# Kernel optimization log

Measured on AMD Instinct MI355X. Metric: run time of the kernel, lower is better.

Reference implementation:

```python
import jax, jax.numpy as jnp
import numpy as np
from jax import lax

DN = ('NCHW', 'OIHW', 'NCHW')

def _attn(x, w):
    # x: [B, C, H, W]; channel pool -> [B, 2, H, W]
    pool = jnp.concatenate([x.max(axis=1, keepdims=True), x.mean(axis=1, keepdims=True)], axis=1)
    g = lax.conv_general_dilated(pool, w, (1, 1), [(3, 3), (3, 3)], dimension_numbers=DN)
    return x * jax.nn.sigmoid(g)

def setup_inputs() -> dict:
    key = jax.random.key(0)
    k0, k1, k2, k3, k4 = jax.random.split(key, 5)
    B, C, H, W = 16, 128, 32, 512
    x = jax.random.normal(k0, (B, C, H, W), dtype=jnp.float32)
    wg = jax.random.normal(k1, (C, C // 2, 1, 3), dtype=jnp.float32) * 0.05  # groups=2 conv weight
    w1 = jax.random.normal(k2, (1, 2, 7, 7), dtype=jnp.float32) * 0.1
    w2 = jax.random.normal(k3, (1, 2, 7, 7), dtype=jnp.float32) * 0.1
    w3 = jax.random.normal(k4, (1, 2, 7, 7), dtype=jnp.float32) * 0.1
    return {"x": x, "wg": wg, "w1": w1, "w2": w2, "w3": w3}

def reference(x, wg, w1, w2, w3):
    # grouped (1,3) conv, padding (0,1), groups=2, no bias
    x = lax.conv_general_dilated(x, wg, (1, 1), [(0, 0), (1, 1)],
                                 dimension_numbers=DN, feature_group_count=2)
    o1 = _attn(x, w1)
    o2 = jnp.transpose(_attn(jnp.transpose(x, (0, 2, 1, 3)), w2), (0, 2, 1, 3))
    o3 = jnp.transpose(_attn(jnp.transpose(x, (0, 3, 2, 1)), w3), (0, 3, 2, 1))
    return (o1 + o2 + o3) / 3.0
```

## Files before the change

kernel.cpp:

```cpp
#include <hip/hip_runtime.h>
#include <math.h>

#define B 16
#define C 128
#define H 32
#define W 512

typedef short bf16x4 __attribute__((ext_vector_type(4)));
typedef short bf16x8 __attribute__((ext_vector_type(8)));
typedef float f32x4 __attribute__((ext_vector_type(4)));

static __device__ inline unsigned short f2bf(float f) {
    unsigned u = __builtin_bit_cast(unsigned, f);
    u += 0x7fffu + ((u >> 16) & 1u);
    return (unsigned short)(u >> 16);
}
static __device__ inline unsigned pack2(float a, float b) {
    unsigned u;
    asm("v_cvt_pk_bf16_f32 %0, %1, %2" : "=v"(u) : "v"(a), "v"(b));
    return u;
}
static __device__ inline float bflo(unsigned u) {
    return __builtin_bit_cast(float, u << 16);
}
static __device__ inline float bfhi(unsigned u) {
    return __builtin_bit_cast(float, u & 0xffff0000u);
}

#define W_FRAGS(wfr, wg, g, wave, col, q)                                      \
    {                                                                          \
        const float* wbase = (wg) + ((size_t)((g) * 64 + (wave) * 16 + (col))) * 192; \
        _Pragma("unroll") for (int tap = 0; tap < 3; ++tap)                    \
            _Pragma("unroll") for (int kk = 0; kk < 2; ++kk) {                 \
                const float* wp = wbase + ((kk) * 32 + (q) * 8) * 3 + tap;     \
                union { unsigned u[4]; bf16x8 v; } pk;                         \
                _Pragma("unroll") for (int e = 0; e < 4; ++e)                  \
                    pk.u[e] = pack2(wp[(2 * e) * 3], wp[(2 * e + 1) * 3]);     \
                wfr[tap][kk] = pk.v;                                           \
            }                                                                  \
    }

__global__ __launch_bounds__(256) void conv_pools(
    const float* __restrict__ x, const float* __restrict__ wg,
    unsigned* __restrict__ pool3p, unsigned* __restrict__ pool1p,
    unsigned* __restrict__ pool2p) {
    __shared__ __align__(16) char xsb[2][34 * 144];
    __shared__ __align__(16) float ytile[2][32][68];

    const int bx = blockIdx.x;
    const int f  = bx & 31;
    const int g  = f & 1;
    const int b  = f >> 1;
    const int chunk = bx >> 5;
    const int wq = chunk >> 1;
    const int hq = chunk & 1;
    const int h0 = hq * 16;
    const int t  = threadIdx.x;
    const int lane = t & 63;
    const int col  = lane & 15;
    const int q    = lane >> 4;
    const int wave = t >> 6;

    bf16x8 wfr[3][2];
    W_FRAGS(wfr, wg, g, wave, col, q);

    float a0[2][4], a1[2][4];
    float hv0 = 0.f, hv1 = 0.f;
    const int w0l = (t & 7) * 4;
    const int ci0 = (t >> 3) * 2;
    const float* xb0 = x + (size_t)(b * C + g * 64 + ci0) * (H * W) + wq * 32 + w0l;
    const int side = (t >> 6) & 1;
    const int hci  = t & 63;
    const int gw   = wq * 32 + (side ? 32 : -1);
    const bool hvalid = (t < 128) && (side ? (wq < 15) : (wq > 0));
    const float* xh0 = x + (size_t)(b * C + g * 64 + hci) * (H * W) + gw;

#define P_LOADX(AA, HVV, h)                                                  \
    {                                                                        \
        const float4 v0 = *(const float4*)(xb0 + (h) * W);                   \
        const float4 v1 = *(const float4*)(xb0 + (size_t)(H * W) + (h) * W); \
        AA[0][0] = v0.x; AA[0][1] = v0.y; AA[0][2] = v0.z; AA[0][3] = v0.w;  \
        AA[1][0] = v1.x; AA[1][1] = v1.y; AA[1][2] = v1.z; AA[1][3] = v1.w;  \
        HVV = hvalid ? xh0[(h) * W] : 0.f;                                   \
    }
#define P_WRITEX(AA, HVV, buf)                                               \
    {                                                                        \
        _Pragma("unroll") for (int j = 0; j < 4; ++j)                        \
            *(unsigned*)((buf) + (size_t)(w0l + j + 1) * 144 + ci0 * 2) =    \
                pack2(AA[0][j], AA[1][j]);                                   \
        if (t < 128)                                                         \
            *(unsigned short*)((buf) + (size_t)(side ? 33 : 0) * 144 +       \
                               hci * 2) = f2bf(HVV);                         \
    }

    f32x4 mH[2], sH[2];
#pragma unroll
    for (int wt = 0; wt < 2; ++wt) {
        mH[wt] = (f32x4){-INFINITY, -INFINITY, -INFINITY, -INFINITY};
        sH[wt] = (f32x4){0.f, 0.f, 0.f, 0.f};
    }

    const int wl = t >> 3;
    const int e  = t & 7;

    P_LOADX(a0, hv0, h0);
    P_WRITEX(a0, hv0, xsb[0]);
    P_LOADX(a1, hv1, h0 + 1);
    P_LOADX(a0, hv0, h0 + 2);
    __syncthreads();

#define P_STEP(hh, CUR, AW, HW, AL, HL)                                        \
    {                                                                          \
        const int h = h0 + (hh);                                               \
        f32x4 acc[2];                                                          \
        acc[0] = (f32x4){0.f, 0.f, 0.f, 0.f};                                  \
        acc[1] = (f32x4){0.f, 0.f, 0.f, 0.f};                                  \
        {                                                                      \
            const char* ab = xsb[CUR] + q * 16;                                \
            _Pragma("unroll") for (int wt = 0; wt < 2; ++wt)                   \
                _Pragma("unroll") for (int kk = 0; kk < 2; ++kk)               \
                    _Pragma("unroll") for (int tap = 0; tap < 3; ++tap) {      \
                        const bf16x8 xf = *(const bf16x8*)(                    \
                            ab + (size_t)(wt * 16 + col + tap) * 144 +         \
                            kk * 64);                                          \
                        acc[wt] = __builtin_amdgcn_mfma_f32_16x16x32_bf16(     \
                            xf, wfr[tap][kk], acc[wt], 0, 0, 0);               \
                    }                                                          \
        }                                                                      \
        _Pragma("unroll") for (int wt = 0; wt < 2; ++wt)                       \
            _Pragma("unroll") for (int r = 0; r < 4; ++r) {                    \
                mH[wt][r] = fmaxf(mH[wt][r], acc[wt][r]);                      \
                sH[wt][r] += acc[wt][r];                                       \
            }                                                                  \
        {                                                                      \
            float m = acc[0][0], s = acc[0][0];                                \
            m = fmaxf(fmaxf(m, acc[0][1]), fmaxf(acc[0][2], acc[0][3]));       \
            s += acc[0][1] + acc[0][2] + acc[0][3];                            \
            _Pragma("unroll") for (int r = 0; r < 4; ++r) {                    \
                m = fmaxf(m, acc[1][r]);                                       \
                s += acc[1][r];                                                \
            }                                                                  \
            m = fmaxf(m, __shfl_xor(m, 16)); s += __shfl_xor(s, 16);           \
            m = fmaxf(m, __shfl_xor(m, 32)); s += __shfl_xor(s, 32);           \
            if (lane < 16)                                                     \
                pool3p[((size_t)(wq * B + b) * H + h) * C + g * 64 +           \
                       wave * 16 + lane] = pack2(m, s);                        \
        }                                                                      \
        _Pragma("unroll") for (int wt = 0; wt < 2; ++wt)                       \
            _Pragma("unroll") for (int r = 0; r < 4; ++r)                      \
                ytile[CUR][wt * 16 + q * 4 + r][wave * 16 + col] = acc[wt][r]; \
        if ((hh) < 15) P_WRITEX(AW, HW, xsb[(CUR) ^ 1]);                       \
        if ((hh) < 13) P_LOADX(AL, HL, h0 + (hh) + 3);                         \
        __syncthreads();                                                       \
        {                                                                      \
            const f32x4 v0 = *(const f32x4*)&ytile[CUR][wl][e * 8];            \
            const f32x4 v1 = *(const f32x4*)&ytile[CUR][wl][e * 8 + 4];        \
            float m = fmaxf(fmaxf(v0[0], v0[1]), fmaxf(v0[2], v0[3]));         \
            float s = v0[0] + v0[1] + v0[2] + v0[3];                           \
            m = fmaxf(m, fmaxf(fmaxf(v1[0], v1[1]), fmaxf(v1[2], v1[3])));     \
            s += v1[0] + v1[1] + v1[2] + v1[3];                                \
            _Pragma("unroll") for (int off = 1; off <= 4; off <<= 1) {         \
                m = fmaxf(m, __shfl_xor(m, off));                              \
                s += __shfl_xor(s, off);                                       \
            }                                                                  \
            if (e == 0)                                                        \
                pool1p[((size_t)(g * B + b) * H + h) * W + wq * 32 + wl] =     \
                    pack2(m, s);                                               \
        }                                                                      \
    }

    for (int hh = 0; hh < 16; hh += 2) {
        P_STEP(hh,     0, a1, hv1, a1, hv1);
        P_STEP(hh + 1, 1, a0, hv0, a0, hv0);
    }
#undef P_STEP

    {
        const int o = g * 64 + wave * 16 + col;
        unsigned* p2 = pool2p + ((size_t)(hq * B + b) * C + o) * W + wq * 32 + q * 4;
#pragma unroll
        for (int wt = 0; wt < 2; ++wt) {
            uint4 pk;
            pk.x = pack2(mH[wt][0], sH[wt][0]);
            pk.y = pack2(mH[wt][1], sH[wt][1]);
            pk.z = pack2(mH[wt][2], sH[wt][2]);
            pk.w = pack2(mH[wt][3], sH[wt][3]);
            *(uint4*)(p2 + wt * 16) = pk;
        }
    }
}

__global__ __launch_bounds__(256) void conv_apply(
    const float* __restrict__ x, const float* __restrict__ wg,
    const float* __restrict__ s1, const float* __restrict__ s2,
    const float* __restrict__ s3, float* __restrict__ out) {
    __shared__ __align__(16) char xsb[2][34 * 144];

    const int bx = blockIdx.x;
    const int f  = bx & 31;
    const int g  = f & 1;
    const int b  = f >> 1;
    const int chunk = bx >> 5;
    const int wq = chunk >> 2;
    const int hq = chunk & 3;
    const int h0 = hq * 8;
    const int t  = threadIdx.x;
    const int lane = t & 63;
    const int col  = lane & 15;
    const int q    = lane >> 4;
    const int wave = t >> 6;

    bf16x8 wfr[3][2];
    W_FRAGS(wfr, wg, g, wave, col, q);

    float a0[2][4], a1[2][4];
    float hv0 = 0.f, hv1 = 0.f;
    const int w0l = (t & 7) * 4;
    const int ci0 = (t >> 3) * 2;
    const float* xb0 = x + (size_t)(b * C + g * 64 + ci0) * (H * W) + wq * 32 + w0l;
    const int side = (t >> 6) & 1;
    const int hci  = t & 63;
    const int gw   = wq * 32 + (side ? 32 : -1);
    const bool hvalid = (t < 128) && (side ? (wq < 15) : (wq > 0));
    const float* xh0 = x + (size_t)(b * C + g * 64 + hci) * (H * W) + gw;

    const int o = g * 64 + wave * 16 + col;
    const float4 g2a = *(const float4*)(s2 + ((size_t)b * C + o) * W + wq * 32 + q * 4);
    const float4 g2b = *(const float4*)(s2 + ((size_t)b * C + o) * W + wq * 32 + q * 4 + 16);

    P_LOADX(a0, hv0, h0);
    P_WRITEX(a0, hv0, xsb[0]);
    P_LOADX(a1, hv1, h0 + 1);
    P_LOADX(a0, hv0, h0 + 2);
    __syncthreads();

#define A_STEP(hh, CUR, AW, HW, AL, HL)                                        \
    {                                                                          \
        const int h = h0 + (hh);                                               \
        f32x4 acc[2];                                                          \
        acc[0] = (f32x4){0.f, 0.f, 0.f, 0.f};                                  \
        acc[1] = (f32x4){0.f, 0.f, 0.f, 0.f};                                  \
        {                                                                      \
            const char* ab = xsb[CUR] + q * 16;                                \
            _Pragma("unroll") for (int wt = 0; wt < 2; ++wt)                   \
                _Pragma("unroll") for (int kk = 0; kk < 2; ++kk)               \
                    _Pragma("unroll") for (int tap = 0; tap < 3; ++tap) {      \
                        const bf16x8 xf = *(const bf16x8*)(                    \
                            ab + (size_t)(wt * 16 + col + tap) * 144 +         \
                            kk * 64);                                          \
                        acc[wt] = __builtin_amdgcn_mfma_f32_16x16x32_bf16(     \
                            xf, wfr[tap][kk], acc[wt], 0, 0, 0);               \
                    }                                                          \
        }                                                                      \
        const float4 g1a =                                                     \
            *(const float4*)(s1 + ((size_t)b * H + h) * W + wq * 32 + q * 4);  \
        const float4 g1b = *(const float4*)(s1 + ((size_t)b * H + h) * W +     \
                                            wq * 32 + q * 4 + 16);             \
        const float g3v = s3[((size_t)b * H + h) * C + o];                     \
        const float k   = 1.f / 3.f;                                           \
        float* ob = out + ((size_t)(b * C + o) * H + h) * W + wq * 32 + q * 4; \
        f32x4 o0, o1;                                                          \
        o0[0] = acc[0][0] * (g1a.x + g2a.x + g3v) * k;                         \
        o0[1] = acc[0][1] * (g1a.y + g2a.y + g3v) * k;                         \
        o0[2] = acc[0][2] * (g1a.z + g2a.z + g3v) * k;                         \
        o0[3] = acc[0][3] * (g1a.w + g2a.w + g3v) * k;                         \
        o1[0] = acc[1][0] * (g1b.x + g2b.x + g3v) * k;                         \
        o1[1] = acc[1][1] * (g1b.y + g2b.y + g3v) * k;                         \
        o1[2] = acc[1][2] * (g1b.z + g2b.z + g3v) * k;                         \
        o1[3] = acc[1][3] * (g1b.w + g2b.w + g3v) * k;                         \
        *(f32x4*)ob        = o0;                                               \
        *(f32x4*)(ob + 16) = o1;                                               \
        if ((hh) < 7) P_WRITEX(AW, HW, xsb[(CUR) ^ 1]);                        \
        if ((hh) < 5) P_LOADX(AL, HL, h0 + (hh) + 3);                          \
        __syncthreads();                                                       \
    }

    for (int hh = 0; hh < 8; hh += 2) {
        A_STEP(hh,     0, a1, hv1, a1, hv1);
        A_STEP(hh + 1, 1, a0, hv0, a0, hv0);
    }
#undef A_STEP
#undef P_LOADX
#undef P_WRITEX
}

__global__ __launch_bounds__(256) void combine(const unsigned* __restrict__ p3p,
                                               float* __restrict__ pool3) {
    const int n = blockIdx.x * 256 + threadIdx.x;
    const int b = n >> 12;
    const int o = n & 4095;
    float m = -INFINITY, s = 0.f;
#pragma unroll
    for (int wq = 0; wq < 16; ++wq) {
        const unsigned u = p3p[(size_t)(wq * B + b) * 4096 + o];
        m = fmaxf(m, bflo(u));
        s += bfhi(u);
    }
    pool3[((size_t)(b * 2 + 0) * H * C) + o] = m;
    pool3[((size_t)(b * 2 + 1) * H * C) + o] = s * (1.f / W);
}

__global__ __launch_bounds__(256) void gates(
    const unsigned* __restrict__ pool1p, const unsigned* __restrict__ pool2p,
    const float* __restrict__ pool3, const float* __restrict__ w1,
    const float* __restrict__ w2, const float* __restrict__ w3,
    float* __restrict__ s1, float* __restrict__ s2, float* __restrict__ s3) {
    const int bid = blockIdx.x;
    if (bid < 256) {
        const int n  = bid * 256 + threadIdx.x;
        const int q0 = (n & 127) * 4;
        const int p  = (n >> 7) & 31;
        const int b  = n >> 12;
        float acc0 = 0.f, acc1 = 0.f, acc2 = 0.f, acc3 = 0.f;
#pragma unroll
        for (int i = 0; i < 7; ++i) {
            const int pp = p + i - 3;
            if (pp < 0 || pp >= H) continue;
            const unsigned* r0 = pool1p + ((size_t)b * H + pp) * W;
            const unsigned* r1 = r0 + 262144;
            float vm[10], vs[10];
#pragma unroll
            for (int j = 0; j < 10; ++j) {
                const int qq = q0 + j - 3;
                const unsigned u0 = (qq >= 0 && qq < W) ? r0[qq] : 0u;
                const unsigned u1 = (qq >= 0 && qq < W) ? r1[qq] : 0u;
                vm[j] = fmaxf(bflo(u0), bflo(u1));
                vs[j] = (bfhi(u0) + bfhi(u1)) * (1.f / C);
            }
            const float* wr0 = w1 + i * 7;
            const float* wr1 = w1 + 49 + i * 7;
#pragma unroll
            for (int j = 0; j < 7; ++j) {
                const float wv0 = wr0[j], wv1 = wr1[j];
                acc0 += vm[j]     * wv0 + vs[j]     * wv1;
                acc1 += vm[j + 1] * wv0 + vs[j + 1] * wv1;
                acc2 += vm[j + 2] * wv0 + vs[j + 2] * wv1;
                acc3 += vm[j + 3] * wv0 + vs[j + 3] * wv1;
            }
        }
        float4 ov;
        ov.x = 1.f / (1.f + expf(-acc0));
        ov.y = 1.f / (1.f + expf(-acc1));
        ov.z = 1.f / (1.f + expf(-acc2));
        ov.w = 1.f / (1.f + expf(-acc3));
        *(float4*)(s1 + (size_t)n * 4) = ov;
    } else if (bid < 1280) {
        const int n  = (bid - 256) * 256 + threadIdx.x;
        const int q0 = (n & 127) * 4;
        const int p  = (n >> 7) & 127;
        const int b  = n >> 14;
        float acc0 = 0.f, acc1 = 0.f, acc2 = 0.f, acc3 = 0.f;
#pragma unroll
        for (int i = 0; i < 7; ++i) {
            const int pp = p + i - 3;
            if (pp < 0 || pp >= C) continue;
            const unsigned* r0 = pool2p + ((size_t)b * C + pp) * W;
            const unsigned* r1 = r0 + 1048576;
            float vm[10], vs[10];
#pragma unroll
            for (int j = 0; j < 10; ++j) {
                const int qq = q0 + j - 3;
                const unsigned u0 = (qq >= 0 && qq < W) ? r0[qq] : 0u;
                const unsigned u1 = (qq >= 0 && qq < W) ? r1[qq] : 0u;
                vm[j] = fmaxf(bflo(u0), bflo(u1));
                vs[j] = (bfhi(u0) + bfhi(u1)) * (1.f / H);
            }
            const float* wr0 = w2 + i * 7;
            const float* wr1 = w2 + 49 + i * 7;
#pragma unroll
            for (int j = 0; j < 7; ++j) {
                const float wv0 = wr0[j], wv1 = wr1[j];
                acc0 += vm[j]     * wv0 + vs[j]     * wv1;
                acc1 += vm[j + 1] * wv0 + vs[j + 1] * wv1;
                acc2 += vm[j + 2] * wv0 + vs[j + 2] * wv1;
                acc3 += vm[j + 3] * wv0 + vs[j + 3] * wv1;
            }
        }
        float4 ov;
        ov.x = 1.f / (1.f + expf(-acc0));
        ov.y = 1.f / (1.f + expf(-acc1));
        ov.z = 1.f / (1.f + expf(-acc2));
        ov.w = 1.f / (1.f + expf(-acc3));
        *(float4*)(s2 + (size_t)n * 4) = ov;
    } else {
        const int n  = (bid - 1280) * 256 + threadIdx.x;
        const int q0 = (n & 31) * 4;
        const int p  = (n >> 5) & 31;
        const int b  = n >> 10;
        float acc0 = 0.f, acc1 = 0.f, acc2 = 0.f, acc3 = 0.f;
#pragma unroll
        for (int c2 = 0; c2 < 2; ++c2) {
#pragma unroll
            for (int i = 0; i < 7; ++i) {
                const int pp = p + i - 3;
                if (pp < 0 || pp >= H) continue;
                const float* row = pool3 + ((size_t)(b * 2 + c2) * H + pp) * C;
                float win[10];
#pragma unroll
                for (int j = 0; j < 10; ++j) {
                    const int qq = q0 + j - 3;
                    win[j] = (qq >= 0 && qq < C) ? row[qq] : 0.f;
                }
                const float* wr = w3 + c2 * 49 + i * 7;
#pragma unroll
                for (int j = 0; j < 7; ++j) {
                    const float wv = wr[j];
                    acc0 += win[j]     * wv;
                    acc1 += win[j + 1] * wv;
                    acc2 += win[j + 2] * wv;
                    acc3 += win[j + 3] * wv;
                }
            }
        }
        float4 ov;
        ov.x = 1.f / (1.f + expf(-acc0));
        ov.y = 1.f / (1.f + expf(-acc1));
        ov.z = 1.f / (1.f + expf(-acc2));
        ov.w = 1.f / (1.f + expf(-acc3));
        *(float4*)(s3 + (size_t)n * 4) = ov;
    }
}

extern "C" void kernel_launch(void* const* d_in, const int* in_sizes, int n_in,
                              void* d_out, int out_size, void* d_ws, size_t ws_size,
                              hipStream_t stream) {
    const float* x  = (const float*)d_in[0];
    const float* wg = (const float*)d_in[1];
    const float* w1 = (const float*)d_in[2];
    const float* w2 = (const float*)d_in[3];
    const float* w3 = (const float*)d_in[4];
    float* out = (float*)d_out;
    float* ws  = (float*)d_ws;

    unsigned* pool1p = (unsigned*)ws;
    unsigned* pool3p = (unsigned*)(ws + 524288);
    unsigned* pool2p = (unsigned*)(ws + 1572864);
    float* pool3 = ws + 3670016;
    float* s1 = ws + 3813376;
    float* s3 = ws + 4075520;
    float* s2 = ws + 524288;

    conv_pools<<<dim3(1024), 256, 0, stream>>>(x, wg, pool3p, pool1p, pool2p);
    combine<<<dim3(256), 256, 0, stream>>>(pool3p, pool3);
    gates<<<dim3(1344), 256, 0, stream>>>(pool1p, pool2p, pool3, w1, w2, w3, s1, s2, s3);
    conv_apply<<<dim3(2048), 256, 0, stream>>>(x, wg, s1, s2, s3, out);
}
```

Measured before the change: 135.8 us.

## Process two rows per barrier phase and pack y tile to bf16 pairs

The conv_pools and apply kernels now handle two h rows per pipeline phase, using double-buffered pairs of x tiles, so there is one __syncthreads per two rows instead of two per row. The per-row channel pool over the y tile is deferred by one phase so it overlaps with the next MFMA compute. The y tile is stored as packed bf16 pairs, which halves its LDS footprint. The cost is double the LDS for x staging, more live registers for two prefetched rows, and slightly lower precision for pool1 inputs.

Measured after the change: 142.6 us. 5.0% more time.

```diff
diff --git a/kernel.cpp b/kernel.cpp
--- a/kernel.cpp
+++ b/kernel.cpp
@@ -6,7 +6,6 @@
 #define H 32
 #define W 512
 
-typedef short bf16x4 __attribute__((ext_vector_type(4)));
 typedef short bf16x8 __attribute__((ext_vector_type(8)));
 typedef float f32x4 __attribute__((ext_vector_type(4)));
 
@@ -40,12 +39,30 @@
             }                                                                  \
     }
 
+#define P_LOADX(AA, HVV, h)                                                  \
+    {                                                                        \
+        const float4 v0 = *(const float4*)(xb0 + (h) * W);                   \
+        const float4 v1 = *(const float4*)(xb0 + (size_t)(H * W) + (h) * W); \
+        AA[0][0] = v0.x; AA[0][1] = v0.y; AA[0][2] = v0.z; AA[0][3] = v0.w;  \
+        AA[1][0] = v1.x; AA[1][1] = v1.y; AA[1][2] = v1.z; AA[1][3] = v1.w;  \
+        HVV = hvalid ? xh0[(h) * W] : 0.f;                                   \
+    }
+#define P_WRITEX(AA, HVV, buf)                                               \
+    {                                                                        \
+        _Pragma("unroll") for (int j = 0; j < 4; ++j)                        \
+            *(unsigned*)((buf) + (size_t)(w0l + j + 1) * 144 + ci0 * 2) =    \
+                pack2(AA[0][j], AA[1][j]);                                   \
+        if (t < 128)                                                         \
+            *(unsigned short*)((buf) + (size_t)(side ? 33 : 0) * 144 +       \
+                               hci * 2) = f2bf(HVV);                         \
+    }
+
 __global__ __launch_bounds__(256) void conv_pools(
     const float* __restrict__ x, const float* __restrict__ wg,
     unsigned* __restrict__ pool3p, unsigned* __restrict__ pool1p,
     unsigned* __restrict__ pool2p) {
-    __shared__ __align__(16) char xsb[2][34 * 144];
-    __shared__ __align__(16) float ytile[2][32][68];
+    __shared__ __align__(16) char xsb[2][2][34 * 144];
+    __shared__ __align__(16) unsigned yt[2][2][16][68];
 
     const int bx = blockIdx.x;
     const int f  = bx & 31;
@@ -64,8 +81,8 @@
     bf16x8 wfr[3][2];
     W_FRAGS(wfr, wg, g, wave, col, q);
 
-    float a0[2][4], a1[2][4];
-    float hv0 = 0.f, hv1 = 0.f;
+    float aA[2][4], aB[2][4];
+    float hvA = 0.f, hvB = 0.f;
     const int w0l = (t & 7) * 4;
     const int ci0 = (t >> 3) * 2;
     const float* xb0 = x + (size_t)(b * C + g * 64 + ci0) * (H * W) + wq * 32 + w0l;
@@ -75,24 +92,6 @@
     const bool hvalid = (t < 128) && (side ? (wq < 15) : (wq > 0));
     const float* xh0 = x + (size_t)(b * C + g * 64 + hci) * (H * W) + gw;
 
-#define P_LOADX(AA, HVV, h)                                                  \
-    {                                                                        \
-        const float4 v0 = *(const float4*)(xb0 + (h) * W);                   \
-        const float4 v1 = *(const float4*)(xb0 + (size_t)(H * W) + (h) * W); \
-        AA[0][0] = v0.x; AA[0][1] = v0.y; AA[0][2] = v0.z; AA[0][3] = v0.w;  \
-        AA[1][0] = v1.x; AA[1][1] = v1.y; AA[1][2] = v1.z; AA[1][3] = v1.w;  \
-        HVV = hvalid ? xh0[(h) * W] : 0.f;                                   \
-    }
-#define P_WRITEX(AA, HVV, buf)                                               \
-    {                                                                        \
-        _Pragma("unroll") for (int j = 0; j < 4; ++j)                        \
-            *(unsigned*)((buf) + (size_t)(w0l + j + 1) * 144 + ci0 * 2) =    \
-                pack2(AA[0][j], AA[1][j]);                                   \
-        if (t < 128)                                                         \
-            *(unsigned short*)((buf) + (size_t)(side ? 33 : 0) * 144 +       \
-                               hci * 2) = f2bf(HVV);                         \
-    }
-
     f32x4 mH[2], sH[2];
 #pragma unroll
     for (int wt = 0; wt < 2; ++wt) {
@@ -100,23 +99,13 @@
         sH[wt] = (f32x4){0.f, 0.f, 0.f, 0.f};
     }
 
-    const int wl = t >> 3;
-    const int e  = t & 7;
-
-    P_LOADX(a0, hv0, h0);
-    P_WRITEX(a0, hv0, xsb[0]);
-    P_LOADX(a1, hv1, h0 + 1);
-    P_LOADX(a0, hv0, h0 + 2);
-    __syncthreads();
-
-#define P_STEP(hh, CUR, AW, HW, AL, HL)                                        \
-    {                                                                          \
-        const int h = h0 + (hh);                                               \
+#define COMPUTEH(h, XBUF, PP, J)                                               \
+    {                                                                          \
         f32x4 acc[2];                                                          \
         acc[0] = (f32x4){0.f, 0.f, 0.f, 0.f};                                  \
         acc[1] = (f32x4){0.f, 0.f, 0.f, 0.f};                                  \
         {                                                                      \
-            const char* ab = xsb[CUR] + q * 16;                                \
+            const char* ab = (XBUF) + q * 16;                                  \
             _Pragma("unroll") for (int wt = 0; wt < 2; ++wt)                   \
                 _Pragma("unroll") for (int kk = 0; kk < 2; ++kk)               \
                     _Pragma("unroll") for (int tap = 0; tap < 3; ++tap) {      \
@@ -143,37 +132,81 @@
             m = fmaxf(m, __shfl_xor(m, 16)); s += __shfl_xor(s, 16);           \
             m = fmaxf(m, __shfl_xor(m, 32)); s += __shfl_xor(s, 32);           \
             if (lane < 16)                                                     \
-                pool3p[((size_t)(wq * B + b) * H + h) * C + g * 64 +           \
+                pool3p[((size_t)(wq * B + b) * H + (h)) * C + g * 64 +         \
                        wave * 16 + lane] = pack2(m, s);                        \
         }                                                                      \
-        _Pragma("unroll") for (int wt = 0; wt < 2; ++wt)                       \
-            _Pragma("unroll") for (int r = 0; r < 4; ++r)                      \
-                ytile[CUR][wt * 16 + q * 4 + r][wave * 16 + col] = acc[wt][r]; \
-        if ((hh) < 15) P_WRITEX(AW, HW, xsb[(CUR) ^ 1]);                       \
-        if ((hh) < 13) P_LOADX(AL, HL, h0 + (hh) + 3);                         \
+        _Pragma("unroll") for (int r = 0; r < 4; ++r)                          \
+            yt[PP][J][q * 4 + r][wave * 16 + col] =                            \
+                pack2(acc[0][r], acc[1][r]);                                   \
+    }
+
+#define POOLC(PP, PAIR)                                                        \
+    {                                                                          \
+        const int j  = t >> 7;                                                 \
+        const int rw = (t & 127) >> 3;                                         \
+        const int e8 = t & 7;                                                  \
+        const unsigned* yr = &yt[PP][j][rw][e8 * 8];                           \
+        const uint4 u0 = *(const uint4*)yr;                                    \
+        const uint4 u1 = *(const uint4*)(yr + 4);                              \
+        float ml = bflo(u0.x), sl = ml, mh = bfhi(u0.x), sh = mh;              \
+        ml = fmaxf(ml, bflo(u0.y)); sl += bflo(u0.y);                          \
+        mh = fmaxf(mh, bfhi(u0.y)); sh += bfhi(u0.y);                          \
+        ml = fmaxf(ml, bflo(u0.z)); sl += bflo(u0.z);                          \
+        mh = fmaxf(mh, bfhi(u0.z)); sh += bfhi(u0.z);                          \
+        ml = fmaxf(ml, bflo(u0.w)); sl += bflo(u0.w);                          \
+        mh = fmaxf(mh, bfhi(u0.w)); sh += bfhi(u0.w);                          \
+        ml = fmaxf(ml, bflo(u1.x)); sl += bflo(u1.x);                          \
+        mh = fmaxf(mh, bfhi(u1.x)); sh += bfhi(u1.x);                          \
+        ml = fmaxf(ml, bflo(u1.y)); sl += bflo(u1.y);                          \
+        mh = fmaxf(mh, bfhi(u1.y)); sh += bfhi(u1.y);                          \
+        ml = fmaxf(ml, bflo(u1.z)); sl += bflo(u1.z);                          \
+        mh = fmaxf(mh, bfhi(u1.z)); sh += bfhi(u1.z);                          \
+        ml = fmaxf(ml, bflo(u1.w)); sl += bflo(u1.w);                          \
+        mh = fmaxf(mh, bfhi(u1.w)); sh += bfhi(u1.w);                          \
+        _Pragma("unroll") for (int off = 1; off <= 4; off <<= 1) {             \
+            ml = fmaxf(ml, __shfl_xor(ml, off)); sl += __shfl_xor(sl, off);    \
+            mh = fmaxf(mh, __shfl_xor(mh, off)); sh += __shfl_xor(sh, off);    \
+        }                                                                      \
+        if (e8 == 0) {                                                         \
+            const int h = h0 + 2 * (PAIR) + j;                                 \
+            unsigned* dst =                                                    \
+                pool1p + ((size_t)(g * B + b) * H + h) * W + wq * 32 + rw;     \
+            dst[0]  = pack2(ml, sl);                                           \
+            dst[16] = pack2(mh, sh);                                           \
+        }                                                                      \
+    }
+
+#define PPHASE(p, P)                                                           \
+    {                                                                          \
+        if ((p) > 0) POOLC((P) ^ 1, (p) - 1);                                  \
+        COMPUTEH(h0 + 2 * (p),     (char*)xsb[P][0], P, 0);                    \
+        COMPUTEH(h0 + 2 * (p) + 1, (char*)xsb[P][1], P, 1);                    \
+        if ((p) < 7) {                                                         \
+            P_WRITEX(aA, hvA, (char*)xsb[(P) ^ 1][0]);                         \
+            P_WRITEX(aB, hvB, (char*)xsb[(P) ^ 1][1]);                         \
+        }                                                                      \
+        if ((p) < 6) {                                                         \
+            P_LOADX(aA, hvA, h0 + 2 * (p) + 4);                                \
+            P_LOADX(aB, hvB, h0 + 2 * (p) + 5);                                \
+        }                                                                      \
         __syncthreads();                                                       \
-        {                                                                      \
-            const f32x4 v0 = *(const f32x4*)&ytile[CUR][wl][e * 8];            \
-            const f32x4 v1 = *(const f32x4*)&ytile[CUR][wl][e * 8 + 4];        \
-            float m = fmaxf(fmaxf(v0[0], v0[1]), fmaxf(v0[2], v0[3]));         \
-            float s = v0[0] + v0[1] + v0[2] + v0[3];                           \
-            m = fmaxf(m, fmaxf(fmaxf(v1[0], v1[1]), fmaxf(v1[2], v1[3])));     \
-            s += v1[0] + v1[1] + v1[2] + v1[3];                                \
-            _Pragma("unroll") for (int off = 1; off <= 4; off <<= 1) {         \
-                m = fmaxf(m, __shfl_xor(m, off));                              \
-                s += __shfl_xor(s, off);                                       \
-            }                                                                  \
-            if (e == 0)                                                        \
-                pool1p[((size_t)(g * B + b) * H + h) * W + wq * 32 + wl] =     \
-                    pack2(m, s);                                               \
-        }                                                                      \
-    }
-
-    for (int hh = 0; hh < 16; hh += 2) {
-        P_STEP(hh,     0, a1, hv1, a1, hv1);
-        P_STEP(hh + 1, 1, a0, hv0, a0, hv0);
-    }
-#undef P_STEP
+    }
+
+    P_LOADX(aA, hvA, h0);
+    P_LOADX(aB, hvB, h0 + 1);
+    P_WRITEX(aA, hvA, (char*)xsb[0][0]);
+    P_WRITEX(aB, hvB, (char*)xsb[0][1]);
+    P_LOADX(aA, hvA, h0 + 2);
+    P_LOADX(aB, hvB, h0 + 3);
+    __syncthreads();
+
+    PPHASE(0, 0); PPHASE(1, 1); PPHASE(2, 0); PPHASE(3, 1);
+    PPHASE(4, 0); PPHASE(5, 1); PPHASE(6, 0); PPHASE(7, 1);
+    POOLC(1, 7);
+
+#undef PPHASE
+#undef POOLC
+#undef COMPUTEH
 
     {
         const int o = g * 64 + wave * 16 + col;
@@ -194,7 +227,7 @@
     const float* __restrict__ x, const float* __restrict__ wg,
     const float* __restrict__ s1, const float* __restrict__ s2,
     const float* __restrict__ s3, float* __restrict__ out) {
-    __shared__ __align__(16) char xsb[2][34 * 144];
+    __shared__ __align__(16) char xsb[2][2][34 * 144];
 
     const int bx = blockIdx.x;
     const int f  = bx & 31;
@@ -213,8 +246,8 @@
     bf16x8 wfr[3][2];
     W_FRAGS(wfr, wg, g, wave, col, q);
 
-    float a0[2][4], a1[2][4];
-    float hv0 = 0.f, hv1 = 0.f;
+    float aA[2][4], aB[2][4];
+    float hvA = 0.f, hvB = 0.f;
     const int w0l = (t & 7) * 4;
     const int ci0 = (t >> 3) * 2;
     const float* xb0 = x + (size_t)(b * C + g * 64 + ci0) * (H * W) + wq * 32 + w0l;
@@ -228,20 +261,13 @@
     const float4 g2a = *(const float4*)(s2 + ((size_t)b * C + o) * W + wq * 32 + q * 4);
     const float4 g2b = *(const float4*)(s2 + ((size_t)b * C + o) * W + wq * 32 + q * 4 + 16);
 
-    P_LOADX(a0, hv0, h0);
-    P_WRITEX(a0, hv0, xsb[0]);
-    P_LOADX(a1, hv1, h0 + 1);
-    P_LOADX(a0, hv0, h0 + 2);
-    __syncthreads();
-
-#define A_STEP(hh, CUR, AW, HW, AL, HL)                                        \
-    {                                                                          \
-        const int h = h0 + (hh);                                               \
+#define ASTEPH(h, XBUF)                                                        \
+    {                                                                          \
         f32x4 acc[2];                                                          \
         acc[0] = (f32x4){0.f, 0.f, 0.f, 0.f};                                  \
         acc[1] = (f32x4){0.f, 0.f, 0.f, 0.f};                                  \
         {                                                                      \
-            const char* ab = xsb[CUR] + q * 16;                                \
+            const char* ab = (XBUF) + q * 16;                                  \
             _Pragma("unroll") for (int wt = 0; wt < 2; ++wt)                   \
                 _Pragma("unroll") for (int kk = 0; kk < 2; ++kk)               \
                     _Pragma("unroll") for (int tap = 0; tap < 3; ++tap) {      \
@@ -252,13 +278,14 @@
                             xf, wfr[tap][kk], acc[wt], 0, 0, 0);               \
                     }                                                          \
         }                                                                      \
-        const float4 g1a =                                                     \
-            *(const float4*)(s1 + ((size_t)b * H + h) * W + wq * 32 + q * 4);  \
-        const float4 g1b = *(const float4*)(s1 + ((size_t)b * H + h) * W +     \
+        const float4 g1a = *(const float4*)(s1 + ((size_t)b * H + (h)) * W +   \
+                                            wq * 32 + q * 4);                  \
+        const float4 g1b = *(const float4*)(s1 + ((size_t)b * H + (h)) * W +   \
                                             wq * 32 + q * 4 + 16);             \
-        const float g3v = s3[((size_t)b * H + h) * C + o];                     \
+        const float g3v = s3[((size_t)b * H + (h)) * C + o];                   \
         const float k   = 1.f / 3.f;                                           \
-        float* ob = out + ((size_t)(b * C + o) * H + h) * W + wq * 32 + q * 4; \
+        float* ob =                                                            \
+            out + ((size_t)(b * C + o) * H + (h)) * W + wq * 32 + q * 4;       \
         f32x4 o0, o1;                                                          \
         o0[0] = acc[0][0] * (g1a.x + g2a.x + g3v) * k;                         \
         o0[1] = acc[0][1] * (g1a.y + g2a.y + g3v) * k;                         \
@@ -270,19 +297,38 @@
         o1[3] = acc[1][3] * (g1b.w + g2b.w + g3v) * k;                         \
         *(f32x4*)ob        = o0;                                               \
         *(f32x4*)(ob + 16) = o1;                                               \
-        if ((hh) < 7) P_WRITEX(AW, HW, xsb[(CUR) ^ 1]);                        \
-        if ((hh) < 5) P_LOADX(AL, HL, h0 + (hh) + 3);                          \
+    }
+
+#define APHASE(p, P)                                                           \
+    {                                                                          \
+        ASTEPH(h0 + 2 * (p),     (char*)xsb[P][0]);                            \
+        ASTEPH(h0 + 2 * (p) + 1, (char*)xsb[P][1]);                            \
+        if ((p) < 3) {                                                         \
+            P_WRITEX(aA, hvA, (char*)xsb[(P) ^ 1][0]);                         \
+            P_WRITEX(aB, hvB, (char*)xsb[(P) ^ 1][1]);                         \
+        }                                                                      \
+        if ((p) < 2) {                                                         \
+            P_LOADX(aA, hvA, h0 + 2 * (p) + 4);                                \
+            P_LOADX(aB, hvB, h0 + 2 * (p) + 5);                                \
+        }                                                                      \
         __syncthreads();                                                       \
     }
 
-    for (int hh = 0; hh < 8; hh += 2) {
-        A_STEP(hh,     0, a1, hv1, a1, hv1);
-        A_STEP(hh + 1, 1, a0, hv0, a0, hv0);
-    }
-#undef A_STEP
+    P_LOADX(aA, hvA, h0);
+    P_LOADX(aB, hvB, h0 + 1);
+    P_WRITEX(aA, hvA, (char*)xsb[0][0]);
+    P_WRITEX(aB, hvB, (char*)xsb[0][1]);
+    P_LOADX(aA, hvA, h0 + 2);
+    P_LOADX(aB, hvB, h0 + 3);
+    __syncthreads();
+
+    APHASE(0, 0); APHASE(1, 1); APHASE(2, 0); APHASE(3, 1);
+
+#undef APHASE
+#undef ASTEPH
+}
 #undef P_LOADX
 #undef P_WRITEX
-}
 
 __global__ __launch_bounds__(256) void combine(const unsigned* __restrict__ p3p,
                                                float* __restrict__ pool3) {
```
